# Performance work log

Measured on AMD Instinct MI355X. Metric: run time of the kernel, lower is better.

The kernel has to match this reference:

```python
import jax, jax.numpy as jnp
import numpy as np

N_FFT = 2048
HOP = 512
PAD = N_FFT // 2  # 1024, center padding
FREQ_BINS = N_FFT // 2 + 1  # 1025


def _fourier_kernels():
    # freq_scale='no', window='hann' (fftbins=True): w[n] = 0.5 - 0.5*cos(2*pi*n/N)
    s = np.arange(N_FFT, dtype=np.float64)
    win = 0.5 - 0.5 * np.cos(2.0 * np.pi * s / N_FFT)
    k = np.arange(FREQ_BINS, dtype=np.float64)[:, None]
    phase = 2.0 * np.pi * k * s[None, :] / N_FFT  # (freq_bins, n_fft)
    wsin = (win[None, :] * np.sin(phase)).astype(np.float32)
    wcos = (win[None, :] * np.cos(phase)).astype(np.float32)
    return wcos, wsin


def setup_inputs() -> dict:
    key = jax.random.key(0)
    x = jax.random.normal(key, (32, 220500), dtype=jnp.float32)
    wcos, wsin = _fourier_kernels()
    return {"x": x, "wcos": jnp.asarray(wcos), "wsin": jnp.asarray(wsin)}


def reference(x, wcos, wsin):
    # x: (B, L). center=True, pad_mode='reflect'
    xp = jnp.pad(x, ((0, 0), (PAD, PAD)), mode="reflect")[:, None, :]  # (B,1,Lp)
    dn = ("NCH", "OIH", "NCH")
    # one conv with both bases stacked -> (B, 2*freq_bins, T)
    kern = jnp.concatenate([wcos, wsin], axis=0)[:, None, :]  # (2F,1,n_fft)
    spec = jax.lax.conv_general_dilated(
        xp, kern, window_strides=(HOP,), padding="VALID", dimension_numbers=dn
    )
    real, imag = spec[:, :FREQ_BINS, :], spec[:, FREQ_BINS:, :]
    # output_format='Complex': stack (real, -imag) on last axis
    return jnp.stack([real, -imag], axis=-1)  # (B, F, T, 2)
```

## Files before the change

### kernel.cpp

```cpp
#include <hip/hip_runtime.h>
#include <hip/hip_bf16.h>

#define L_IN   220500
#define PADK   1024
#define LP     222548
#define LPP    222560
#define BATCH  32
#define HOPSZ  512
#define T_FR   431
#define F_BINS 1025
#define M_TOT  (BATCH * T_FR)
#define N_GEMM 2048
#define K_TOT  2048
#define NT_K   64
#define GEMM_BLOCKS 864
#define NYQ_BLOCKS  48
#define XBLOCKS 3488
#define WBLOCKS 2048

typedef short short8 __attribute__((ext_vector_type(8)));
typedef float floatx4 __attribute__((ext_vector_type(4)));

__device__ __forceinline__ void glds16(const void* g, void* l) {
    __builtin_amdgcn_global_load_lds(
        (const __attribute__((address_space(1))) void*)g,
        (__attribute__((address_space(3))) void*)l, 16, 0, 0);
}

__device__ __forceinline__ short f2bf(float f) {
    __hip_bfloat16 h = __float2bfloat16(f);
    return *reinterpret_cast<short*>(&h);
}

__global__ void k_prep(const float* __restrict__ x,
                       const float* __restrict__ wcos, const float* __restrict__ wsin,
                       __hip_bfloat16* __restrict__ xp, __hip_bfloat16* __restrict__ wb) {
    int blk = blockIdx.x;
    if (blk < XBLOCKS) {
        int b = blk / 109, ix = blk - b * 109;
        int i0 = (ix * 256 + threadIdx.x) * 8;
        if (i0 >= LP) return;
        const float* xb = x + (size_t)b * L_IN;
        __hip_bfloat16* xpb = xp + (size_t)b * LPP;
        if (i0 >= PADK && i0 + 8 <= PADK + L_IN) {
            const float4* s4 = (const float4*)(xb + (i0 - PADK));
            float4 a = s4[0], d = s4[1];
            short8 o;
            o[0]=f2bf(a.x); o[1]=f2bf(a.y); o[2]=f2bf(a.z); o[3]=f2bf(a.w);
            o[4]=f2bf(d.x); o[5]=f2bf(d.y); o[6]=f2bf(d.z); o[7]=f2bf(d.w);
            *(short8*)((short*)xpb + i0) = o;
        } else {
            for (int u = 0; u < 8; ++u) {
                int i = i0 + u;
                if (i >= LP) break;
                int j = i - PADK;
                if (j < 0) j = -j;
                if (j >= L_IN) j = 2 * L_IN - 2 - j;
                xpb[i] = __float2bfloat16(xb[j]);
            }
        }
    } else {
        int i0 = ((blk - XBLOCKS) * 256 + threadIdx.x) * 8;
        int np = i0 >> 11;
        int k  = i0 & (K_TOT - 1);
        int kf = np >> 1;
        const float* src = ((np & 1) ? wsin : wcos) + (size_t)kf * K_TOT + k;
        float4 a = ((const float4*)src)[0], d = ((const float4*)src)[1];
        short8 o;
        o[0]=f2bf(a.x); o[1]=f2bf(a.y); o[2]=f2bf(a.z); o[3]=f2bf(a.w);
        o[4]=f2bf(d.x); o[5]=f2bf(d.y); o[6]=f2bf(d.z); o[7]=f2bf(d.w);
        *(short8*)((short*)wb + i0) = o;
    }
}

#define BARRIER { asm volatile("" ::: "memory"); __builtin_amdgcn_s_barrier(); asm volatile("" ::: "memory"); }
#define VMW(N)  asm volatile("s_waitcnt vmcnt(" #N ")" ::: "memory")
#define SGB(M,N) __builtin_amdgcn_sched_group_barrier((M), (N), 0)
#define SP1     __builtin_amdgcn_s_setprio(1)
#define SP0     __builtin_amdgcn_s_setprio(0)

__global__ __launch_bounds__(512, 4) void k_gemm(
    const __hip_bfloat16* __restrict__ xp,
    const __hip_bfloat16* __restrict__ wb,
    const float* __restrict__ wcos,
    float* __restrict__ out) {

    __shared__ short lds[36864];

    const int tid  = threadIdx.x;
    const int wave = tid >> 6;
    const int lane = tid & 63;

    if (blockIdx.x >= GEMM_BLOCKS) {
        const int gw = (blockIdx.x - GEMM_BLOCKS) * 8 + wave;
        const float* wr = wcos + (size_t)1024 * K_TOT;
        for (int f = gw; f < M_TOT; f += NYQ_BLOCKS * 8) {
            int b = f / T_FR, t = f - b * T_FR;
            const __hip_bfloat16* xr = xp + (size_t)b * LPP + t * HOPSZ;
            float sum = 0.f;
            #pragma unroll
            for (int i = 0; i < 4; ++i) {
                int s = i * 512 + lane * 8;
                short8 xv = *(const short8*)((const short*)xr + s);
                const float4* wv = (const float4*)(wr + s);
                float4 w0 = wv[0], w1 = wv[1];
                float xs[8];
                #pragma unroll
                for (int u = 0; u < 8; ++u)
                    xs[u] = __uint_as_float(((unsigned)(unsigned short)xv[u]) << 16);
                sum += xs[0]*w0.x + xs[1]*w0.y + xs[2]*w0.z + xs[3]*w0.w
                     + xs[4]*w1.x + xs[5]*w1.y + xs[6]*w1.z + xs[7]*w1.w;
            }
            #pragma unroll
            for (int off = 32; off > 0; off >>= 1) sum += __shfl_xor(sum, off);
            if (lane == 0) {
                float2 v; v.x = sum; v.y = 0.f;
                ((float2*)out)[((size_t)b * F_BINS + 1024) * T_FR + t] = v;
            }
        }
        return;
    }

    const int quad  = lane >> 4;
    const int l15   = lane & 15;
    const int waveM = wave >> 2;
    const int waveN = wave & 3;

    const int bn = blockIdx.x & 7;
    const int bm = blockIdx.x >> 3;

    const int l4 = lane >> 2, lc = lane & 3;
    const int swz = (lc ^ ((l4 >> 1) & 3)) * 8;
    int am = bm * 128 + wave * 16 + l4;
    if (am > M_TOT - 1) am = M_TOT - 1;
    const int ab_ = am / T_FR, at_ = am - ab_ * T_FR;
    const int aoff  = ab_ * LPP + at_ * HOPSZ + swz;
    const int bnrow = bn * 256 + wave * 32 + l4;
    const int boff0 = bnrow * K_TOT + swz;
    const int boff1 = (bnrow + 16) * K_TOT + swz;
    const int adst  = wave * 512;
    const int bdst  = wave * 1024;

    const int rchunk = (quad ^ ((l15 >> 1) & 3)) * 8;
    const int ara = (waveM * 64 + l15) * 32 + rchunk;
    const int bra = (waveN * 64 + l15) * 32 + rchunk;

#define STAGE(BUF, K0) { \
        glds16(xp + aoff  + (K0), &lds[(BUF) * 4096 + adst]); \
        glds16(wb + boff0 + (K0), &lds[12288 + (BUF) * 8192 + bdst]); \
        glds16(wb + boff1 + (K0), &lds[12288 + (BUF) * 8192 + bdst + 512]); }

    short8 xf[4], wf[4];
    floatx4 acc[4][4] = {};

    STAGE(0, 0);
    STAGE(1, 32);
    VMW(3);
    BARRIER;

    int r0 = 0, r1 = 1, r2 = 2;
    #pragma unroll 1
    for (int t = 0; t < NT_K; ++t) {
        if (t < NT_K - 2) STAGE(r2, (t + 2) * 32);
        if (t < NT_K - 2)      { VMW(3); }
        else if (t == NT_K - 2){ VMW(0); }
        SP1;
        wf[0] = *(const short8*)&lds[12288 + r0 * 8192 + bra];
        #pragma unroll
        for (int j = 0; j < 4; ++j)
            xf[j] = *(const short8*)&lds[r0 * 4096 + ara + j * 512];
        #pragma unroll
        for (int i = 1; i < 4; ++i)
            wf[i] = *(const short8*)&lds[12288 + r0 * 8192 + bra + i * 512];
        #pragma unroll
        for (int i = 0; i < 4; ++i)
            #pragma unroll
            for (int j = 0; j < 4; ++j)
                acc[i][j] = __builtin_amdgcn_mfma_f32_16x16x32_bf16(wf[i], xf[j], acc[i][j], 0, 0, 0);
        SGB(0x100, 2); SGB(0x8, 1);
        SGB(0x100, 1); SGB(0x8, 1);
        SGB(0x100, 1); SGB(0x8, 1);
        SGB(0x100, 1); SGB(0x8, 1);
        SGB(0x100, 1); SGB(0x8, 4);
        SGB(0x100, 1); SGB(0x8, 4);
        SGB(0x100, 1); SGB(0x8, 4);
        SP0;
        if (t < NT_K - 1) BARRIER;
        int tmp = r0; r0 = r1; r1 = r2; r2 = tmp;
    }

    float2* __restrict__ out2 = (float2*)out;
    #pragma unroll
    for (int j = 0; j < 4; ++j) {
        int m = bm * 128 + waveM * 64 + j * 16 + l15;
        if (m >= M_TOT) continue;
        int b = m / T_FR, t = m - b * T_FR;
        long tbase = (long)b * (F_BINS * T_FR) + t;
        #pragma unroll
        for (int i = 0; i < 4; ++i) {
            int nb = bn * 256 + waveN * 64 + i * 16 + quad * 4;
            #pragma unroll
            for (int p = 0; p < 2; ++p) {
                int k = (nb + 2 * p) >> 1;
                float2 v; v.x = acc[i][j][2 * p]; v.y = -acc[i][j][2 * p + 1];
                out2[tbase + (long)k * T_FR] = v;
            }
        }
    }
}

extern "C" void kernel_launch(void* const* d_in, const int* in_sizes, int n_in,
                              void* d_out, int out_size, void* d_ws, size_t ws_size,
                              hipStream_t stream) {
    const float* x    = (const float*)d_in[0];
    const float* wcos = (const float*)d_in[1];
    const float* wsin = (const float*)d_in[2];
    float* out = (float*)d_out;

    __hip_bfloat16* xp = (__hip_bfloat16*)d_ws;
    __hip_bfloat16* wb = (__hip_bfloat16*)((char*)d_ws + (size_t)BATCH * LPP * sizeof(__hip_bfloat16));

    k_prep<<<XBLOCKS + WBLOCKS, 256, 0, stream>>>(x, wcos, wsin, xp, wb);
    k_gemm<<<GEMM_BLOCKS + NYQ_BLOCKS, 512, 0, stream>>>(xp, wb, wcos, out);
}
```

Measured before the change: 270.6 us.

## Apply radix-4 decimation to split the STFT DFT GEMM into smaller sub-GEMMs

The prep kernel now windows each frame and folds its four 512-sample quarters into butterfly combinations (sum, alternating sum, real and imaginary difference pairs). Frequency bins are thereby partitioned by k mod 4 into sub-problems with K of 512 or 1024 instead of 2048, which roughly halves the MFMA work. The twiddle bases are regenerated on the GPU with sincos instead of being converted from the wcos/wsin inputs. The change also drops the scheduling group barriers, remaps the block order and lowers launch bounds occupancy. It adds a materialised per-frame buffer and computes the basis functions itself, which changes bf16 rounding relative to the provided kernels.

```diff
diff --git a/kernel.cpp b/kernel.cpp
--- a/kernel.cpp
+++ b/kernel.cpp
@@ -2,21 +2,17 @@
 #include <hip/hip_bf16.h>
 
 #define L_IN   220500
-#define PADK   1024
-#define LP     222548
-#define LPP    222560
 #define BATCH  32
-#define HOPSZ  512
 #define T_FR   431
 #define F_BINS 1025
 #define M_TOT  (BATCH * T_FR)
-#define N_GEMM 2048
-#define K_TOT  2048
-#define NT_K   64
+#define KROW   2048
+#define WG02   524288
+#define WG1    1048576
 #define GEMM_BLOCKS 864
 #define NYQ_BLOCKS  48
-#define XBLOCKS 3488
-#define WBLOCKS 2048
+#define BF_BLOCKS   1728
+#define WGT_BLOCKS  384
 
 typedef short short8 __attribute__((ext_vector_type(8)));
 typedef float floatx4 __attribute__((ext_vector_type(4)));
@@ -32,123 +28,158 @@
     return *reinterpret_cast<short*>(&h);
 }
 
-__global__ void k_prep(const float* __restrict__ x,
-                       const float* __restrict__ wcos, const float* __restrict__ wsin,
-                       __hip_bfloat16* __restrict__ xp, __hip_bfloat16* __restrict__ wb) {
-    int blk = blockIdx.x;
-    if (blk < XBLOCKS) {
-        int b = blk / 109, ix = blk - b * 109;
-        int i0 = (ix * 256 + threadIdx.x) * 8;
-        if (i0 >= LP) return;
+__global__ __launch_bounds__(512) void k_prep(const float* __restrict__ x,
+        const float* __restrict__ wcos,
+        __hip_bfloat16* __restrict__ yb, __hip_bfloat16* __restrict__ w2) {
+    const int blk = blockIdx.x, tid = threadIdx.x;
+    if (blk < BF_BLOCKS) {
+        int b = blk / 54, rem = blk - b * 54;
+        int t = rem * 8 + (tid >> 6);
+        if (t >= T_FR) return;
+        int q = (tid & 63) * 8;
         const float* xb = x + (size_t)b * L_IN;
-        __hip_bfloat16* xpb = xp + (size_t)b * LPP;
-        if (i0 >= PADK && i0 + 8 <= PADK + L_IN) {
-            const float4* s4 = (const float4*)(xb + (i0 - PADK));
-            float4 a = s4[0], d = s4[1];
-            short8 o;
-            o[0]=f2bf(a.x); o[1]=f2bf(a.y); o[2]=f2bf(a.z); o[3]=f2bf(a.w);
-            o[4]=f2bf(d.x); o[5]=f2bf(d.y); o[6]=f2bf(d.z); o[7]=f2bf(d.w);
-            *(short8*)((short*)xpb + i0) = o;
+        float a[4][8];
+        #pragma unroll
+        for (int p = 0; p < 4; ++p) {
+            const float4* wv = (const float4*)(wcos + 512 * p + q);
+            float4 w0 = wv[0], w1 = wv[1];
+            float w[8] = {w0.x,w0.y,w0.z,w0.w,w1.x,w1.y,w1.z,w1.w};
+            int jb = t * 512 + 512 * p + q - 1024;
+            if (jb >= 0 && jb <= L_IN - 8) {
+                const float4* s4 = (const float4*)(xb + jb);
+                float4 v0 = s4[0], v1 = s4[1];
+                float v[8] = {v0.x,v0.y,v0.z,v0.w,v1.x,v1.y,v1.z,v1.w};
+                #pragma unroll
+                for (int u = 0; u < 8; ++u) a[p][u] = v[u] * w[u];
+            } else {
+                #pragma unroll
+                for (int u = 0; u < 8; ++u) {
+                    int j = jb + u;
+                    if (j < 0) j = -j;
+                    if (j >= L_IN) j = 2 * L_IN - 2 - j;
+                    a[p][u] = xb[j] * w[u];
+                }
+            }
+        }
+        short8 y0, y2, yre, yim;
+        #pragma unroll
+        for (int u = 0; u < 8; ++u) {
+            y0[u]  = f2bf(a[0][u] + a[1][u] + a[2][u] + a[3][u]);
+            y2[u]  = f2bf(a[0][u] - a[1][u] + a[2][u] - a[3][u]);
+            yre[u] = f2bf(a[0][u] - a[2][u]);
+            yim[u] = f2bf(a[3][u] - a[1][u]);
+        }
+        short* yr = (short*)yb + (size_t)(b * T_FR + t) * KROW;
+        *(short8*)(yr + q)        = y0;
+        *(short8*)(yr + 512 + q)  = y2;
+        *(short8*)(yr + 1024 + q) = yre;
+        *(short8*)(yr + 1536 + q) = yim;
+    } else {
+        long e0 = (long)(blk - BF_BLOCKS) * 4096 + (long)tid * 8;
+        short8 o;
+        const float SC = 3.0679615757712823e-3f;
+        if (e0 < WG02) {
+            int n = (int)(e0 >> 9), q0 = (int)(e0 & 511);
+            int c = n & 1;
+            int k = (n < 512) ? 4 * (n >> 1) : 4 * ((n - 512) >> 1) + 2;
+            #pragma unroll
+            for (int u = 0; u < 8; ++u) {
+                int ph = (k * (q0 + u)) & 2047;
+                float s, cc;
+                __sincosf((float)ph * SC, &s, &cc);
+                o[u] = f2bf(c ? -s : cc);
+            }
         } else {
+            long f = e0 - WG02;
+            int n = (int)(f >> 10), q0 = (int)(f & 1023);
+            int c = n & 1, v = n >> 1;
+            int half = q0 >> 9, qq = q0 & 511;
+            int k = (v < 256) ? 4 * v + 1 : 3069 - 4 * v;
+            #pragma unroll
             for (int u = 0; u < 8; ++u) {
-                int i = i0 + u;
-                if (i >= LP) break;
-                int j = i - PADK;
-                if (j < 0) j = -j;
-                if (j >= L_IN) j = 2 * L_IN - 2 - j;
-                xpb[i] = __float2bfloat16(xb[j]);
-            }
-        }
-    } else {
-        int i0 = ((blk - XBLOCKS) * 256 + threadIdx.x) * 8;
-        int np = i0 >> 11;
-        int k  = i0 & (K_TOT - 1);
-        int kf = np >> 1;
-        const float* src = ((np & 1) ? wsin : wcos) + (size_t)kf * K_TOT + k;
-        float4 a = ((const float4*)src)[0], d = ((const float4*)src)[1];
-        short8 o;
-        o[0]=f2bf(a.x); o[1]=f2bf(a.y); o[2]=f2bf(a.z); o[3]=f2bf(a.w);
-        o[4]=f2bf(d.x); o[5]=f2bf(d.y); o[6]=f2bf(d.z); o[7]=f2bf(d.w);
-        *(short8*)((short*)wb + i0) = o;
+                int ph = (k * (qq + u)) & 2047;
+                float s, cc;
+                __sincosf((float)ph * SC, &s, &cc);
+                float val;
+                if (v < 256) val = c ? (half ? cc : -s) : (half ? s : cc);
+                else         val = c ? (half ? -cc : s) : (half ? s : cc);
+                o[u] = f2bf(val);
+            }
+        }
+        *(short8*)((short*)w2 + e0) = o;
     }
 }
 
 #define BARRIER { asm volatile("" ::: "memory"); __builtin_amdgcn_s_barrier(); asm volatile("" ::: "memory"); }
 #define VMW(N)  asm volatile("s_waitcnt vmcnt(" #N ")" ::: "memory")
-#define SGB(M,N) __builtin_amdgcn_sched_group_barrier((M), (N), 0)
 #define SP1     __builtin_amdgcn_s_setprio(1)
 #define SP0     __builtin_amdgcn_s_setprio(0)
 
-__global__ __launch_bounds__(512, 4) void k_gemm(
-    const __hip_bfloat16* __restrict__ xp,
-    const __hip_bfloat16* __restrict__ wb,
-    const float* __restrict__ wcos,
+__global__ __launch_bounds__(512, 2) void k_gemm(
+    const __hip_bfloat16* __restrict__ yb,
+    const __hip_bfloat16* __restrict__ w2,
     float* __restrict__ out) {
 
     __shared__ short lds[36864];
-
-    const int tid  = threadIdx.x;
-    const int wave = tid >> 6;
-    const int lane = tid & 63;
+    const int tid = threadIdx.x, wave = tid >> 6, lane = tid & 63;
 
     if (blockIdx.x >= GEMM_BLOCKS) {
         const int gw = (blockIdx.x - GEMM_BLOCKS) * 8 + wave;
-        const float* wr = wcos + (size_t)1024 * K_TOT;
         for (int f = gw; f < M_TOT; f += NYQ_BLOCKS * 8) {
-            int b = f / T_FR, t = f - b * T_FR;
-            const __hip_bfloat16* xr = xp + (size_t)b * LPP + t * HOPSZ;
+            const short* yr = (const short*)yb + (size_t)f * KROW;
+            short8 v = *(const short8*)(yr + lane * 8);
             float sum = 0.f;
             #pragma unroll
-            for (int i = 0; i < 4; ++i) {
-                int s = i * 512 + lane * 8;
-                short8 xv = *(const short8*)((const short*)xr + s);
-                const float4* wv = (const float4*)(wr + s);
-                float4 w0 = wv[0], w1 = wv[1];
-                float xs[8];
-                #pragma unroll
-                for (int u = 0; u < 8; ++u)
-                    xs[u] = __uint_as_float(((unsigned)(unsigned short)xv[u]) << 16);
-                sum += xs[0]*w0.x + xs[1]*w0.y + xs[2]*w0.z + xs[3]*w0.w
-                     + xs[4]*w1.x + xs[5]*w1.y + xs[6]*w1.z + xs[7]*w1.w;
+            for (int u = 0; u < 8; ++u) {
+                float e = __uint_as_float(((unsigned)(unsigned short)v[u]) << 16);
+                sum += (u & 1) ? -e : e;
             }
             #pragma unroll
             for (int off = 32; off > 0; off >>= 1) sum += __shfl_xor(sum, off);
             if (lane == 0) {
-                float2 v; v.x = sum; v.y = 0.f;
-                ((float2*)out)[((size_t)b * F_BINS + 1024) * T_FR + t] = v;
+                int b = f / T_FR, t = f - b * T_FR;
+                float2 o; o.x = sum; o.y = 0.f;
+                ((float2*)out)[((size_t)b * F_BINS + 1024) * T_FR + t] = o;
             }
         }
         return;
     }
 
-    const int quad  = lane >> 4;
-    const int l15   = lane & 15;
-    const int waveM = wave >> 2;
-    const int waveN = wave & 3;
-
-    const int bn = blockIdx.x & 7;
-    const int bm = blockIdx.x >> 3;
+    const int bi = blockIdx.x;
+    const int bm = (bi & 3) + ((bi >> 5) << 2);
+    const int bn = (bi >> 2) & 7;
+
+    const int quad = lane >> 4, l15 = lane & 15;
+    const int waveM = wave >> 2, waveN = wave & 3;
+
+    const int g1f   = bn >> 2;
+    const int Kg    = g1f ? 1024 : 512;
+    const int NTt   = g1f ? 32 : 16;
+    const int Koff  = (bn < 2) ? 0 : (bn < 4 ? 512 : 1024);
+    const long bbase= g1f ? (long)WG02 + (long)(bn - 4) * 256 * 1024
+                          : (long)bn * 256 * 512;
+    const int kind  = (bn < 2) ? 0 : (bn < 4 ? 2 : 1);
+    const int bnl   = (bn < 2) ? bn : (bn < 4 ? bn - 2 : bn - 4);
 
     const int l4 = lane >> 2, lc = lane & 3;
     const int swz = (lc ^ ((l4 >> 1) & 3)) * 8;
     int am = bm * 128 + wave * 16 + l4;
     if (am > M_TOT - 1) am = M_TOT - 1;
-    const int ab_ = am / T_FR, at_ = am - ab_ * T_FR;
-    const int aoff  = ab_ * LPP + at_ * HOPSZ + swz;
-    const int bnrow = bn * 256 + wave * 32 + l4;
-    const int boff0 = bnrow * K_TOT + swz;
-    const int boff1 = (bnrow + 16) * K_TOT + swz;
-    const int adst  = wave * 512;
-    const int bdst  = wave * 1024;
+    const int aoff  = am * KROW + Koff + swz;
+    const int brl   = wave * 32 + l4;
+    const long boff0 = bbase + (long)brl * Kg + swz;
+    const long boff1 = boff0 + (long)16 * Kg;
+    const int adst = wave * 512;
+    const int bdst = wave * 1024;
 
     const int rchunk = (quad ^ ((l15 >> 1) & 3)) * 8;
     const int ara = (waveM * 64 + l15) * 32 + rchunk;
     const int bra = (waveN * 64 + l15) * 32 + rchunk;
 
 #define STAGE(BUF, K0) { \
-        glds16(xp + aoff  + (K0), &lds[(BUF) * 4096 + adst]); \
-        glds16(wb + boff0 + (K0), &lds[12288 + (BUF) * 8192 + bdst]); \
-        glds16(wb + boff1 + (K0), &lds[12288 + (BUF) * 8192 + bdst + 512]); }
+        glds16(yb + aoff  + (K0), &lds[(BUF) * 4096 + adst]); \
+        glds16(w2 + boff0 + (K0), &lds[12288 + (BUF) * 8192 + bdst]); \
+        glds16(w2 + boff1 + (K0), &lds[12288 + (BUF) * 8192 + bdst + 512]); }
 
     short8 xf[4], wf[4];
     floatx4 acc[4][4] = {};
@@ -160,10 +191,10 @@
 
     int r0 = 0, r1 = 1, r2 = 2;
     #pragma unroll 1
-    for (int t = 0; t < NT_K; ++t) {
-        if (t < NT_K - 2) STAGE(r2, (t + 2) * 32);
-        if (t < NT_K - 2)      { VMW(3); }
-        else if (t == NT_K - 2){ VMW(0); }
+    for (int t = 0; t < NTt; ++t) {
+        if (t < NTt - 2) STAGE(r2, (t + 2) * 32);
+        if (t < NTt - 2)      { VMW(3); }
+        else if (t == NTt - 2){ VMW(0); }
         SP1;
         wf[0] = *(const short8*)&lds[12288 + r0 * 8192 + bra];
         #pragma unroll
@@ -177,15 +208,8 @@
             #pragma unroll
             for (int j = 0; j < 4; ++j)
                 acc[i][j] = __builtin_amdgcn_mfma_f32_16x16x32_bf16(wf[i], xf[j], acc[i][j], 0, 0, 0);
-        SGB(0x100, 2); SGB(0x8, 1);
-        SGB(0x100, 1); SGB(0x8, 1);
-        SGB(0x100, 1); SGB(0x8, 1);
-        SGB(0x100, 1); SGB(0x8, 1);
-        SGB(0x100, 1); SGB(0x8, 4);
-        SGB(0x100, 1); SGB(0x8, 4);
-        SGB(0x100, 1); SGB(0x8, 4);
         SP0;
-        if (t < NT_K - 1) BARRIER;
+        if (t < NTt - 1) BARRIER;
         int tmp = r0; r0 = r1; r1 = r2; r2 = tmp;
     }
 
@@ -195,15 +219,17 @@
         int m = bm * 128 + waveM * 64 + j * 16 + l15;
         if (m >= M_TOT) continue;
         int b = m / T_FR, t = m - b * T_FR;
-        long tbase = (long)b * (F_BINS * T_FR) + t;
+        long tb = (long)b * (F_BINS * T_FR) + t;
         #pragma unroll
         for (int i = 0; i < 4; ++i) {
-            int nb = bn * 256 + waveN * 64 + i * 16 + quad * 4;
             #pragma unroll
             for (int p = 0; p < 2; ++p) {
-                int k = (nb + 2 * p) >> 1;
-                float2 v; v.x = acc[i][j][2 * p]; v.y = -acc[i][j][2 * p + 1];
-                out2[tbase + (long)k * T_FR] = v;
+                int pi = bnl * 128 + waveN * 32 + i * 8 + quad * 2 + p;
+                int k = (kind == 0) ? 4 * pi
+                      : (kind == 2) ? 4 * pi + 2
+                      : (pi < 256 ? 4 * pi + 1 : 4 * pi - 1021);
+                float2 v; v.x = acc[i][j][2 * p]; v.y = acc[i][j][2 * p + 1];
+                out2[tb + (long)k * T_FR] = v;
             }
         }
     }
@@ -214,12 +240,11 @@
                               hipStream_t stream) {
     const float* x    = (const float*)d_in[0];
     const float* wcos = (const float*)d_in[1];
-    const float* wsin = (const float*)d_in[2];
     float* out = (float*)d_out;
 
-    __hip_bfloat16* xp = (__hip_bfloat16*)d_ws;
-    __hip_bfloat16* wb = (__hip_bfloat16*)((char*)d_ws + (size_t)BATCH * LPP * sizeof(__hip_bfloat16));
-
-    k_prep<<<XBLOCKS + WBLOCKS, 256, 0, stream>>>(x, wcos, wsin, xp, wb);
-    k_gemm<<<GEMM_BLOCKS + NYQ_BLOCKS, 512, 0, stream>>>(xp, wb, wcos, out);
-}
+    __hip_bfloat16* yb = (__hip_bfloat16*)d_ws;
+    __hip_bfloat16* w2 = (__hip_bfloat16*)((char*)d_ws + (size_t)M_TOT * KROW * 2);
+
+    k_prep<<<BF_BLOCKS + WGT_BLOCKS, 512, 0, stream>>>(x, wcos, yb, w2);
+    k_gemm<<<GEMM_BLOCKS + NYQ_BLOCKS, 512, 0, stream>>>(yb, w2, out);
+}
```

After: 223.6 us. -17.4%, faster.
